# Kernel optimization log

Measured on AMD Instinct MI355X. Metric: run time of the kernel, lower is better.

Reference implementation:

```python
import jax, jax.numpy as jnp
import numpy as np

T_LEN = 1024
N_IN = 512
BATCH = 32
SURR_ALPHA = 4.0  # slope of the sigmoid surrogate gradient


@jax.custom_vjp
def heaviside_sg(x):
    # spike = Heaviside(x); backward uses sigmoid surrogate derivative
    return (x >= 0).astype(x.dtype)

def _hs_fwd(x):
    return heaviside_sg(x), x

def _hs_bwd(x, g):
    s = jax.nn.sigmoid(SURR_ALPHA * x)
    return (g * SURR_ALPHA * s * (1.0 - s),)

heaviside_sg.defvjp(_hs_fwd, _hs_bwd)


def setup_inputs() -> dict:
    key = jax.random.key(0)
    k1, k2, k3 = jax.random.split(key, 3)
    current = jax.random.normal(k1, (T_LEN, BATCH, N_IN), dtype=jnp.float32)
    beta = jax.random.uniform(k2, (N_IN,), dtype=jnp.float32)  # per-channel decay in (0,1)
    v_init = jax.random.normal(k3, (BATCH, N_IN), dtype=jnp.float32)
    v_th = jnp.ones((T_LEN, BATCH, N_IN), dtype=jnp.float32)
    return {"current": current, "beta": beta, "v_init": v_init, "v_th": v_th}


def reference(current, beta, v_init, v_th):
    # Torch version: grouped causal conv1d with kernel beta^{T-1-k}, i.e.
    # membrane[t] = sum_{j<=t} beta^{t-j} * current[j], with current[0] += beta*v_init.
    # Equivalent O(T) linear recurrence: m_t = beta*m_{t-1} + c_t, m_{-1}=v_init.
    def step(m, c):
        m = beta * m + c  # beta (N,) broadcasts over (B,N)
        return m, m

    m_last, membrane = jax.lax.scan(step, v_init, current)  # membrane: (T,B,N)

    # surrogate-gradient spike function
    spikes = heaviside_sg(membrane - v_th)  # (T,B,N)

    # triangular phi kernel: z[t] = sum_{j<=t} (t-j+1)*spikes[j] == double cumsum
    z = jnp.cumsum(jnp.cumsum(spikes, axis=0), axis=0)  # (T,B,N)

    # Block.g: keep entries equal to 1, zero everything else; gradient is identity
    # (the subtracted term is detached in the torch code).
    gz = z - jax.lax.stop_gradient(jnp.where(z == 1.0, 0.0, z))

    return gz, z, m_last  # m_last == membrane[:, :, -1] in torch layout (B,N)
```

## Files before the change

### kernel.cpp

```cpp
#include <hip/hip_runtime.h>


#define T_LEN 1024
#define N_IN  512
#define BN    16384
#define DW    (T_LEN / 32)

#define CHB   256
#define NBLK1 (BN / CHB)
#define SEGT  16
#define NSEG1 (T_LEN / SEGT)
#define RING1 4
#define TPAD  17

__global__ __launch_bounds__(768, 1) void snn_scan_wide(
        const float* __restrict__ cur, const float* __restrict__ beta,
        const float* __restrict__ vini, const float* __restrict__ vth,
        unsigned* __restrict__ bitsg, unsigned* __restrict__ Pc,
        float* __restrict__ ml)
{
    __shared__ float stage[2 * RING1 * CHB * TPAD];
    __shared__ volatile int prod[2][RING1];
    __shared__ volatile int scons[4];

    const int lane   = threadIdx.x & 63;
    const int wave   = threadIdx.x >> 6;
    const int chbase = blockIdx.x * CHB;

    if (threadIdx.x < 8)  prod[threadIdx.x & 1][threadIdx.x >> 1] = 0;
    if (threadIdx.x < 4)  scons[threadIdx.x] = 0;
    __syncthreads();

    if (wave >= 4) {
        const int w = wave - 4;
        const int a = w & 1;
        const int r = w >> 1;
        const float* __restrict__ src = (a == 0) ? cur : vth;

        for (int s = r; s < NSEG1; s += RING1) {
            if (s >= RING1) {
                const int need = s - RING1 + 1;
                while (scons[0] < need || scons[1] < need ||
                       scons[2] < need || scons[3] < need)
                    __builtin_amdgcn_s_sleep(1);
                asm volatile("" ::: "memory");
            }
            float4 rg[SEGT];
#pragma unroll
            for (int t = 0; t < SEGT; ++t)
                rg[t] = *reinterpret_cast<const float4*>(
                            src + (size_t)(s * SEGT + t) * BN + chbase + 4 * lane);
            float* base = &stage[((a * RING1 + (s & (RING1 - 1))) * CHB
                                  + 4 * lane) * TPAD];
#pragma unroll
            for (int t = 0; t < SEGT; ++t) {
                base[0 * TPAD + t] = rg[t].x;
                base[1 * TPAD + t] = rg[t].y;
                base[2 * TPAD + t] = rg[t].z;
                base[3 * TPAD + t] = rg[t].w;
            }
            asm volatile("s_waitcnt lgkmcnt(0)" ::: "memory");
            prod[a][s & (RING1 - 1)] = s + 1;
        }
    } else {
        const int i = chbase + 64 * wave + lane;
        const int chl = 64 * wave + lane;
        const float bta = beta[i & (N_IN - 1)];
        float m = vini[i];
        int C = 0, Z = 0;
        unsigned mlo = 0u;

        const float* cbase = &stage[(0 * RING1 * CHB + chl) * TPAD];
        const float* vbase = &stage[(1 * RING1 * CHB + chl) * TPAD];

#pragma unroll 1
        for (int s = 0; s < NSEG1; ++s) {
            const int sl = s & (RING1 - 1);
            while (prod[0][sl] < s + 1 || prod[1][sl] < s + 1)
                __builtin_amdgcn_s_sleep(1);
            asm volatile("" ::: "memory");

            if ((s & 1) == 0)
                Pc[(size_t)(s >> 1) * BN + i] = (unsigned)C | ((unsigned)Z << 11);

            const float* lc = cbase + sl * CHB * TPAD;
            const float* lv = vbase + sl * CHB * TPAD;
            float cc[SEGT], vv[SEGT];
#pragma unroll
            for (int t = 0; t < SEGT; ++t) { cc[t] = lc[t]; vv[t] = lv[t]; }

            unsigned mask = 0u;
#pragma unroll
            for (int t = 0; t < SEGT; ++t) {
                m = fmaf(bta, m, cc[t]);
                const int sp = (m >= vv[t]) ? 1 : 0;
                mask |= (unsigned)sp << t;
                C += sp;
                Z += C;
            }
            if ((s & 1) == 0) {
                mlo = mask;
            } else {
                bitsg[(size_t)(s >> 1) * BN + i] = mlo | (mask << 16);
            }
            asm volatile("s_waitcnt lgkmcnt(0)" ::: "memory");
            if (lane == 0) scons[wave] = s + 1;
        }
        ml[i] = m;
    }
}

__global__ __launch_bounds__(256, 4) void snn_expand(
        const unsigned* __restrict__ bitsg, const unsigned* __restrict__ Pc,
        float* __restrict__ gz, float* __restrict__ zo)
{
    const int d  = blockIdx.x & (DW - 1);
    const int cb = blockIdx.x / DW;
    const int cg = threadIdx.x & 63;
    const int tt = threadIdx.x >> 6;
    const int ch = cb * 256 + cg * 4;

    const uint4 u  = *reinterpret_cast<const uint4*>(&bitsg[(size_t)d * BN + ch]);
    const uint4 p4 = *reinterpret_cast<const uint4*>(&Pc[(size_t)d * BN + ch]);
    int C0 = (int)(p4.x & 0x7FFu), Z0 = (int)(p4.x >> 11);
    int C1 = (int)(p4.y & 0x7FFu), Z1 = (int)(p4.y >> 11);
    int C2 = (int)(p4.z & 0x7FFu), Z2 = (int)(p4.z >> 11);
    int C3 = (int)(p4.w & 0x7FFu), Z3 = (int)(p4.w >> 11);

    const int pre = tt * 8;
    for (int b = 0; b < pre; ++b) {
        C0 += (int)((u.x >> b) & 1u); Z0 += C0;
        C1 += (int)((u.y >> b) & 1u); Z1 += C1;
        C2 += (int)((u.z >> b) & 1u); Z2 += C2;
        C3 += (int)((u.w >> b) & 1u); Z3 += C3;
    }

    float* __restrict__ gp = gz + (size_t)(d * 32 + pre) * BN + ch;
    float* __restrict__ zp = zo + (size_t)(d * 32 + pre) * BN + ch;
#pragma unroll
    for (int r = 0; r < 8; ++r) {
        const int b = pre + r;
        C0 += (int)((u.x >> b) & 1u); Z0 += C0;
        C1 += (int)((u.y >> b) & 1u); Z1 += C1;
        C2 += (int)((u.z >> b) & 1u); Z2 += C2;
        C3 += (int)((u.w >> b) & 1u); Z3 += C3;
        const float4 gf = make_float4(Z0 == 1 ? 1.0f : 0.0f,
                                      Z1 == 1 ? 1.0f : 0.0f,
                                      Z2 == 1 ? 1.0f : 0.0f,
                                      Z3 == 1 ? 1.0f : 0.0f);
        const float4 zf = make_float4((float)Z0, (float)Z1,
                                      (float)Z2, (float)Z3);
        *reinterpret_cast<float4*>(gp + (size_t)r * BN) = gf;
        *reinterpret_cast<float4*>(zp + (size_t)r * BN) = zf;
    }
}

#define U 16
struct Buf { float c[U]; float v[U]; };

__device__ __forceinline__ void prefetch(Buf& b, const float* __restrict__ cp,
                                         const float* __restrict__ vp, int t0) {
    if (t0 >= T_LEN) return;
    const float* __restrict__ c = cp + (size_t)t0 * BN;
    const float* __restrict__ v = vp + (size_t)t0 * BN;
#pragma unroll
    for (int u = 0; u < U; ++u) {
        b.c[u] = c[(size_t)u * BN];
        b.v[u] = v[(size_t)u * BN];
    }
}

__device__ __forceinline__ unsigned process16(const Buf& b, float beta, float& m) {
    unsigned mask = 0u;
#pragma unroll
    for (int u = 0; u < U; ++u) {
        m = fmaf(beta, m, b.c[u]);
        mask |= (m >= b.v[u]) ? (1u << u) : 0u;
    }
    return mask;
}

__global__ __launch_bounds__(512, 2) void snn_fused_fb(
        const float* __restrict__ cur, const float* __restrict__ beta,
        const float* __restrict__ vini, const float* __restrict__ vth,
        float* __restrict__ gz, float* __restrict__ zo, float* __restrict__ ml)
{
    __shared__ unsigned bits[T_LEN / 32][64];
    const int lane = threadIdx.x & 63;
    const int wave = threadIdx.x >> 6;
    const int i = blockIdx.x * 64 + lane;

    if (wave == 0) {
        const float bta = beta[i & (N_IN - 1)];
        float m = vini[i];
        const float* cp = cur + i;
        const float* vp = vth + i;
        Buf b0, b1, b2, b3;
        prefetch(b0, cp, vp, 0);     prefetch(b1, cp, vp, U);
        prefetch(b2, cp, vp, 2 * U); prefetch(b3, cp, vp, 3 * U);
        for (int t0 = 0; t0 < T_LEN; t0 += 4 * U) {
            unsigned m0 = process16(b0, bta, m); prefetch(b0, cp, vp, t0 + 4 * U);
            unsigned m1 = process16(b1, bta, m); prefetch(b1, cp, vp, t0 + 5 * U);
            bits[t0 >> 5][lane] = m0 | (m1 << 16);
            unsigned m2 = process16(b2, bta, m); prefetch(b2, cp, vp, t0 + 6 * U);
            unsigned m3 = process16(b3, bta, m); prefetch(b3, cp, vp, t0 + 7 * U);
            bits[(t0 >> 5) + 1][lane] = m2 | (m3 << 16);
        }
        ml[i] = m;
    }
    __syncthreads();

    int C = 0, Z = 0;
    const int d0 = wave * 4;
    for (int d = 0; d < d0; ++d) {
        unsigned u = bits[d][lane];
#pragma unroll
        for (int b = 0; b < 32; ++b) { C += (u >> b) & 1u; Z += C; }
    }
    float* __restrict__ gp = gz + (size_t)(d0 * 32) * BN + i;
    float* __restrict__ zp = zo + (size_t)(d0 * 32) * BN + i;
    for (int d = 0; d < 4; ++d) {
        unsigned u = bits[d0 + d][lane];
#pragma unroll
        for (int b = 0; b < 32; ++b) {
            C += (u >> b) & 1u;
            Z += C;
            const size_t off = (size_t)(d * 32 + b) * BN;
            gp[off] = (Z == 1) ? 1.0f : 0.0f;
            zp[off] = (float)Z;
        }
    }
}

extern "C" void kernel_launch(void* const* d_in, const int* in_sizes, int n_in,
                              void* d_out, int out_size, void* d_ws, size_t ws_size,
                              hipStream_t stream) {
    const float* cur  = (const float*)d_in[0];
    const float* beta = (const float*)d_in[1];
    const float* vini = (const float*)d_in[2];
    const float* vth  = (const float*)d_in[3];
    float* gz = (float*)d_out;
    float* zo = gz + (size_t)T_LEN * BN;
    float* ml = zo + (size_t)T_LEN * BN;

    const size_t need = (size_t)DW * BN * sizeof(unsigned) * 2;

    if (d_ws != nullptr && ws_size >= need) {
        unsigned* bitsg = (unsigned*)d_ws;
        unsigned* Pc = bitsg + (size_t)DW * BN;
        snn_scan_wide<<<NBLK1, 768, 0, stream>>>(cur, beta, vini, vth,
                                                 bitsg, Pc, ml);
        snn_expand<<<DW * (BN / 256), 256, 0, stream>>>(bitsg, Pc, gz, zo);
    } else {
        snn_fused_fb<<<BN / 64, 512, 0, stream>>>(cur, beta, vini, vth,
                                                  gz, zo, ml);
    }
}
```

Measured before the change: 267.3 us.

## Restructure scan kernel into 64-channel blocks with direct global-to-LDS async loads

The scan kernel now runs one compute wave per 64-channel block, with two producer waves (one for current, one for threshold) feeding an 8-deep LDS ring. The producers use global_load_lds, which writes global memory straight into LDS and skips the register round-trip and the padded transpose store. They keep several segments in flight and signal readiness through vmcnt waits. This gives 256 blocks instead of 64 for more CU coverage and deeper memory pipelining, at the cost of low occupancy per block and spin waits that now carry an iteration cap.

```diff
diff --git a/kernel.cpp b/kernel.cpp
--- a/kernel.cpp
+++ b/kernel.cpp
@@ -6,105 +6,100 @@
 #define BN    16384
 #define DW    (T_LEN / 32)
 
-#define CHB   256
-#define NBLK1 (BN / CHB)
-#define SEGT  16
-#define NSEG1 (T_LEN / SEGT)
-#define RING1 4
-#define TPAD  17
-
-__global__ __launch_bounds__(768, 1) void snn_scan_wide(
+#define P1_SEGT 16
+#define P1_NSEG (T_LEN / P1_SEGT)
+#define P1_RING 8
+#define P1_DEP  3
+
+#define SPIN_WHILE(cond) do { unsigned _g = 0;                               \
+        while ((cond) && (++_g < (1u << 18))) __builtin_amdgcn_s_sleep(1);   \
+        asm volatile("" ::: "memory"); } while (0)
+
+__device__ __forceinline__ void gload_lds16(const float* g, float* l) {
+    __builtin_amdgcn_global_load_lds(
+        (const __attribute__((address_space(1))) void*)g,
+        (__attribute__((address_space(3))) void*)l, 16, 0, 0);
+}
+
+__global__ __launch_bounds__(192, 1) void snn_scan3(
         const float* __restrict__ cur, const float* __restrict__ beta,
         const float* __restrict__ vini, const float* __restrict__ vth,
         unsigned* __restrict__ bitsg, unsigned* __restrict__ Pc,
         float* __restrict__ ml)
 {
-    __shared__ float stage[2 * RING1 * CHB * TPAD];
-    __shared__ volatile int prod[2][RING1];
-    __shared__ volatile int scons[4];
+    __shared__ float ldsC[P1_RING][P1_SEGT * 64];
+    __shared__ float ldsV[P1_RING][P1_SEGT * 64];
+    __shared__ volatile int prodC, prodV, consS;
 
     const int lane   = threadIdx.x & 63;
     const int wave   = threadIdx.x >> 6;
-    const int chbase = blockIdx.x * CHB;
-
-    if (threadIdx.x < 8)  prod[threadIdx.x & 1][threadIdx.x >> 1] = 0;
-    if (threadIdx.x < 4)  scons[threadIdx.x] = 0;
+    const int chbase = blockIdx.x * 64;
+
+    if (threadIdx.x == 0) { prodC = 0; prodV = 0; consS = 0; }
     __syncthreads();
 
-    if (wave >= 4) {
-        const int w = wave - 4;
-        const int a = w & 1;
-        const int r = w >> 1;
-        const float* __restrict__ src = (a == 0) ? cur : vth;
-
-        for (int s = r; s < NSEG1; s += RING1) {
-            if (s >= RING1) {
-                const int need = s - RING1 + 1;
-                while (scons[0] < need || scons[1] < need ||
-                       scons[2] < need || scons[3] < need)
-                    __builtin_amdgcn_s_sleep(1);
-                asm volatile("" ::: "memory");
+    if (wave >= 1) {
+        const float* __restrict__ src = (wave == 1) ? cur : vth;
+        float* ring = (wave == 1) ? &ldsC[0][0] : &ldsV[0][0];
+        volatile int* prod = (wave == 1) ? &prodC : &prodV;
+        const size_t goff = (size_t)chbase + (size_t)(lane >> 4) * BN
+                          + (size_t)(4 * (lane & 15));
+
+#pragma unroll 1
+        for (int s = 0; s < P1_NSEG; ++s) {
+            if (s >= P1_RING)
+                SPIN_WHILE(consS < s - P1_RING + 1);
+            float* dst = ring + (s & (P1_RING - 1)) * (P1_SEGT * 64);
+#pragma unroll
+            for (int j = 0; j < P1_SEGT / 4; ++j)
+                gload_lds16(src + (size_t)(s * P1_SEGT + 4 * j) * BN + goff,
+                            dst + j * 256);
+            if (s >= P1_DEP) {
+                asm volatile("s_waitcnt vmcnt(12)" ::: "memory");
+                *prod = s - P1_DEP + 1;
             }
-            float4 rg[SEGT];
-#pragma unroll
-            for (int t = 0; t < SEGT; ++t)
-                rg[t] = *reinterpret_cast<const float4*>(
-                            src + (size_t)(s * SEGT + t) * BN + chbase + 4 * lane);
-            float* base = &stage[((a * RING1 + (s & (RING1 - 1))) * CHB
-                                  + 4 * lane) * TPAD];
-#pragma unroll
-            for (int t = 0; t < SEGT; ++t) {
-                base[0 * TPAD + t] = rg[t].x;
-                base[1 * TPAD + t] = rg[t].y;
-                base[2 * TPAD + t] = rg[t].z;
-                base[3 * TPAD + t] = rg[t].w;
-            }
-            asm volatile("s_waitcnt lgkmcnt(0)" ::: "memory");
-            prod[a][s & (RING1 - 1)] = s + 1;
-        }
+        }
+        asm volatile("s_waitcnt vmcnt(8)" ::: "memory"); *prod = P1_NSEG - 2;
+        asm volatile("s_waitcnt vmcnt(4)" ::: "memory"); *prod = P1_NSEG - 1;
+        asm volatile("s_waitcnt vmcnt(0)" ::: "memory"); *prod = P1_NSEG;
     } else {
-        const int i = chbase + 64 * wave + lane;
-        const int chl = 64 * wave + lane;
+        const int i = chbase + lane;
         const float bta = beta[i & (N_IN - 1)];
         float m = vini[i];
         int C = 0, Z = 0;
         unsigned mlo = 0u;
 
-        const float* cbase = &stage[(0 * RING1 * CHB + chl) * TPAD];
-        const float* vbase = &stage[(1 * RING1 * CHB + chl) * TPAD];
-
 #pragma unroll 1
-        for (int s = 0; s < NSEG1; ++s) {
-            const int sl = s & (RING1 - 1);
-            while (prod[0][sl] < s + 1 || prod[1][sl] < s + 1)
-                __builtin_amdgcn_s_sleep(1);
-            asm volatile("" ::: "memory");
+        for (int s = 0; s < P1_NSEG; ++s) {
+            SPIN_WHILE(prodC < s + 1 || prodV < s + 1);
+            const int sl = s & (P1_RING - 1);
+            const float* lc = &ldsC[sl][lane];
+            const float* lv = &ldsV[sl][lane];
 
             if ((s & 1) == 0)
-                Pc[(size_t)(s >> 1) * BN + i] = (unsigned)C | ((unsigned)Z << 11);
-
-            const float* lc = cbase + sl * CHB * TPAD;
-            const float* lv = vbase + sl * CHB * TPAD;
-            float cc[SEGT], vv[SEGT];
-#pragma unroll
-            for (int t = 0; t < SEGT; ++t) { cc[t] = lc[t]; vv[t] = lv[t]; }
-
+                Pc[(size_t)(s >> 1) * BN + i] =
+                    (unsigned)C | ((unsigned)Z << 11);
+
+            float cc[P1_SEGT], vv[P1_SEGT];
+#pragma unroll
+            for (int t = 0; t < P1_SEGT; ++t) {
+                cc[t] = lc[t * 64];
+                vv[t] = lv[t * 64];
+            }
             unsigned mask = 0u;
 #pragma unroll
-            for (int t = 0; t < SEGT; ++t) {
+            for (int t = 0; t < P1_SEGT; ++t) {
                 m = fmaf(bta, m, cc[t]);
                 const int sp = (m >= vv[t]) ? 1 : 0;
                 mask |= (unsigned)sp << t;
                 C += sp;
                 Z += C;
             }
-            if ((s & 1) == 0) {
-                mlo = mask;
-            } else {
-                bitsg[(size_t)(s >> 1) * BN + i] = mlo | (mask << 16);
-            }
+            if ((s & 1) == 0) mlo = mask;
+            else bitsg[(size_t)(s >> 1) * BN + i] = mlo | (mask << 16);
+
             asm volatile("s_waitcnt lgkmcnt(0)" ::: "memory");
-            if (lane == 0) scons[wave] = s + 1;
+            if (lane == 0) consS = s + 1;
         }
         ml[i] = m;
     }
@@ -248,8 +243,8 @@
     if (d_ws != nullptr && ws_size >= need) {
         unsigned* bitsg = (unsigned*)d_ws;
         unsigned* Pc = bitsg + (size_t)DW * BN;
-        snn_scan_wide<<<NBLK1, 768, 0, stream>>>(cur, beta, vini, vth,
-                                                 bitsg, Pc, ml);
+        snn_scan3<<<BN / 64, 192, 0, stream>>>(cur, beta, vini, vth,
+                                               bitsg, Pc, ml);
         snn_expand<<<DW * (BN / 256), 256, 0, stream>>>(bitsg, Pc, gz, zo);
     } else {
         snn_fused_fb<<<BN / 64, 512, 0, stream>>>(cur, beta, vini, vth,
```

Measured after the change: 253.5 us. 5.2% less time.
